# Performance work log

Hardware: AMD Instinct MI355X
Metric: run time of the kernel (lower is better)

The kernel has to match this reference:

```python
import jax, jax.numpy as jnp
import numpy as np

B, M, I = 32, 8192, 256
TEMPERATURE = 1.0


def setup_inputs() -> dict:
    key = jax.random.key(0)
    k1, k2, k3, k4 = jax.random.split(key, 4)
    memory = jax.random.normal(k1, (B, M, I), dtype=jnp.float32)
    qkey = jax.random.normal(k2, (B, I), dtype=jnp.float32)
    beta = jax.random.uniform(k3, (B,), dtype=jnp.float32)
    # xavier-uniform init for Linear(I, I)
    limit = float(np.sqrt(6.0 / (I + I)))
    W = jax.random.uniform(k4, (I, I), dtype=jnp.float32, minval=-limit, maxval=limit)
    b = jnp.zeros((I,), dtype=jnp.float32)
    return {"memory": memory, "key": qkey, "beta": beta, "W": W, "b": b}


def reference(memory, key, beta, W, b):
    # projected_key = tanh(key @ W^T + b)  -- torch Linear stores weight [out, in]
    projected_key = jnp.tanh(key @ W.T + b)                      # [B, I]
    diff = projected_key[:, None, :] - memory                    # [B, M, I]
    distances = jnp.sum(diff * diff, axis=-1)                    # [B, M]
    similarity = -distances
    weights = jax.nn.softmax(beta[:, None] * similarity / TEMPERATURE, axis=-1)  # [B, M]
    read_vector = jnp.einsum('bm,bmi->bi', weights, memory)      # [B, I]
    return weights, read_vector, similarity
```

## Files before the change

kernel.cpp:

```cpp
#include <hip/hip_runtime.h>
#include <math.h>

constexpr int Bdim = 32;
constexpr int Mdim = 8192;
constexpr int Idim = 256;
constexpr int ROWS_PER_BLOCK = 128;
constexpr int ROWS_PER_WAVE = 32;
constexpr int NCHUNK = Mdim / ROWS_PER_BLOCK;
constexpr int NSLICE = 8;

__global__ void proj_key_kernel(const float* __restrict__ key,
                                const float* __restrict__ W,
                                const float* __restrict__ bias,
                                float* __restrict__ pk) {
    int b = blockIdx.x >> 3;
    int slice = blockIdx.x & 7;
    int tid = threadIdx.x;
    int row = slice * 32 + (tid >> 3);
    int seg = tid & 7;

    const float4* w4 = (const float4*)(W + (size_t)row * Idim) + seg * 8;
    const float4* k4 = (const float4*)(key + (size_t)b * Idim) + seg * 8;
    float s = 0.f;
    #pragma unroll
    for (int k = 0; k < 8; ++k) {
        float4 wv = w4[k];
        float4 kv = k4[k];
        s += wv.x * kv.x + wv.y * kv.y + wv.z * kv.z + wv.w * kv.w;
    }
    s += __shfl_xor(s, 4, 64);
    s += __shfl_xor(s, 2, 64);
    s += __shfl_xor(s, 1, 64);
    if (seg == 0) pk[(size_t)b * Idim + row] = tanhf(s + bias[row]);
}

__global__ void fused_pass1_kernel(const float* __restrict__ memory,
                                   const float* __restrict__ pk,
                                   const float* __restrict__ beta,
                                   float* __restrict__ sim,
                                   float* __restrict__ pvec,
                                   float* __restrict__ pmx,
                                   float* __restrict__ psum) {
    int b = blockIdx.x / NCHUNK;
    int c = blockIdx.x % NCHUNK;
    int wave = threadIdx.x >> 6;
    int lane = threadIdx.x & 63;
    float bt = beta[b];

    float4 pkv = ((const float4*)(pk + (size_t)b * Idim))[lane];

    int row0 = c * ROWS_PER_BLOCK + wave * ROWS_PER_WAVE;
    const float* base = memory + ((size_t)b * Mdim + row0) * Idim;
    float* simp = sim + (size_t)b * Mdim + row0;

    float mx = -INFINITY, ssum = 0.f;
    float4 acc = make_float4(0.f, 0.f, 0.f, 0.f);
    float my_sim = 0.f;

    const float4* rp = (const float4*)base + lane;

    for (int g = 0; g < ROWS_PER_WAVE / 8; ++g) {
        float4 m[8];
        #pragma unroll
        for (int j = 0; j < 8; ++j)
            m[j] = rp[(size_t)(g * 8 + j) * 64];

        float s[8];
        #pragma unroll
        for (int j = 0; j < 8; ++j) {
            float dx = pkv.x - m[j].x, dy = pkv.y - m[j].y;
            float dz = pkv.z - m[j].z, dw = pkv.w - m[j].w;
            s[j] = dx * dx + dy * dy + dz * dz + dw * dw;
        }
        #pragma unroll
        for (int off = 32; off; off >>= 1) {
            #pragma unroll
            for (int j = 0; j < 8; ++j) s[j] += __shfl_xor(s[j], off, 64);
        }
        if ((lane >> 3) == g) my_sim = -s[lane & 7];

        #pragma unroll
        for (int j = 0; j < 8; ++j) s[j] = -bt * s[j];
        float gm = fmaxf(fmaxf(fmaxf(s[0], s[1]), fmaxf(s[2], s[3])),
                         fmaxf(fmaxf(s[4], s[5]), fmaxf(s[6], s[7])));
        if (gm > mx) {
            float sc = __expf(mx - gm);
            ssum *= sc;
            acc.x *= sc; acc.y *= sc; acc.z *= sc; acc.w *= sc;
            mx = gm;
        }
        float ps = 0.f;
        #pragma unroll
        for (int j = 0; j < 8; ++j) {
            float p = __expf(s[j] - mx);
            ps += p;
            acc.x = fmaf(p, m[j].x, acc.x);
            acc.y = fmaf(p, m[j].y, acc.y);
            acc.z = fmaf(p, m[j].z, acc.z);
            acc.w = fmaf(p, m[j].w, acc.w);
        }
        ssum += ps;
    }
    if (lane < 32) simp[lane] = my_sim;

    __shared__ float lacc[4][Idim];
    __shared__ float lmx[4], lsum[4];
    ((float4*)lacc[wave])[lane] = acc;
    if (lane == 0) { lmx[wave] = mx; lsum[wave] = ssum; }
    __syncthreads();

    float MX = fmaxf(fmaxf(lmx[0], lmx[1]), fmaxf(lmx[2], lmx[3]));
    float e0 = __expf(lmx[0] - MX), e1 = __expf(lmx[1] - MX);
    float e2 = __expf(lmx[2] - MX), e3 = __expf(lmx[3] - MX);
    int i = threadIdx.x;
    float v = lacc[0][i] * e0 + lacc[1][i] * e1 + lacc[2][i] * e2 + lacc[3][i] * e3;
    size_t pc = (size_t)b * NCHUNK + c;
    pvec[pc * Idim + i] = v;
    if (threadIdx.x == 0) {
        pmx[pc] = MX;
        psum[pc] = lsum[0] * e0 + lsum[1] * e1 + lsum[2] * e2 + lsum[3] * e3;
    }
}

__global__ void epilogue_kernel(const float* __restrict__ pvec,
                                const float* __restrict__ pmx,
                                const float* __restrict__ psum,
                                const float* __restrict__ sim,
                                const float* __restrict__ beta,
                                float* __restrict__ read_vec,
                                float* __restrict__ weights) {
    int b = blockIdx.x / NSLICE;
    int slice = blockIdx.x % NSLICE;
    int tid = threadIdx.x;
    __shared__ float e[NCHUNK];
    __shared__ float MXs, sInvs;

    if (tid < NCHUNK) {
        float m = pmx[(size_t)b * NCHUNK + tid];
        float mm = m;
        #pragma unroll
        for (int off = 32; off; off >>= 1) mm = fmaxf(mm, __shfl_xor(mm, off, 64));
        float ec = __expf(m - mm);
        e[tid] = ec;
        float sc = psum[(size_t)b * NCHUNK + tid] * ec;
        #pragma unroll
        for (int off = 32; off; off >>= 1) sc += __shfl_xor(sc, off, 64);
        if (tid == 0) { MXs = mm; sInvs = 1.f / sc; }
    }
    __syncthreads();

    float MX = MXs, inv = sInvs;

    if (slice == 0) {
        float v = 0.f;
        const float* p = pvec + (size_t)b * NCHUNK * Idim + tid;
        #pragma unroll 8
        for (int c = 0; c < NCHUNK; ++c) v += p[(size_t)c * Idim] * e[c];
        read_vec[(size_t)b * Idim + tid] = v * inv;
    }

    float bt = beta[b];
    int m4 = slice * (Mdim / NSLICE / 4) + tid;
    float4 s = ((const float4*)(sim + (size_t)b * Mdim))[m4];
    float4 w;
    w.x = __expf(bt * s.x - MX) * inv;
    w.y = __expf(bt * s.y - MX) * inv;
    w.z = __expf(bt * s.z - MX) * inv;
    w.w = __expf(bt * s.w - MX) * inv;
    ((float4*)(weights + (size_t)b * Mdim))[m4] = w;
}

extern "C" void kernel_launch(void* const* d_in, const int* in_sizes, int n_in,
                              void* d_out, int out_size, void* d_ws, size_t ws_size,
                              hipStream_t stream) {
    const float* memory = (const float*)d_in[0];
    const float* key    = (const float*)d_in[1];
    const float* beta   = (const float*)d_in[2];
    const float* W      = (const float*)d_in[3];
    const float* bias   = (const float*)d_in[4];

    float* out = (float*)d_out;
    float* weights  = out;
    float* read_vec = out + (size_t)Bdim * Mdim;
    float* sim      = read_vec + (size_t)Bdim * Idim;

    float* pk   = (float*)d_ws;
    float* pvec = pk + (size_t)Bdim * Idim;
    float* pmx  = pvec + (size_t)Bdim * NCHUNK * Idim;
    float* psum = pmx + (size_t)Bdim * NCHUNK;

    proj_key_kernel<<<Bdim * 8, 256, 0, stream>>>(key, W, bias, pk);
    fused_pass1_kernel<<<Bdim * NCHUNK, 256, 0, stream>>>(memory, pk, beta,
                                                          sim, pvec, pmx, psum);
    epilogue_kernel<<<Bdim * NSLICE, 256, 0, stream>>>(pvec, pmx, psum, sim, beta,
                                                       read_vec, weights);
}
```

Measured before the change: 53.90 us.

## Fuse softmax epilogue into main pass via last-block atomic counter

Merges the separate epilogue kernel into the main streaming kernel. Each block increments a per-batch atomic counter after writing its partials, and the last block for each batch performs the cross-chunk max/sum combine, the read vector, and the weights normalisation. This removes one kernel launch and its dependency gap. In exchange it adds a memset of the counters and serialises the weights tail onto 32 blocks instead of 256.

```diff
diff --git a/kernel.cpp b/kernel.cpp
--- a/kernel.cpp
+++ b/kernel.cpp
@@ -7,7 +7,6 @@
 constexpr int ROWS_PER_BLOCK = 128;
 constexpr int ROWS_PER_WAVE = 32;
 constexpr int NCHUNK = Mdim / ROWS_PER_BLOCK;
-constexpr int NSLICE = 8;
 
 __global__ void proj_key_kernel(const float* __restrict__ key,
                                 const float* __restrict__ W,
@@ -34,17 +33,21 @@
     if (seg == 0) pk[(size_t)b * Idim + row] = tanhf(s + bias[row]);
 }
 
-__global__ void fused_pass1_kernel(const float* __restrict__ memory,
-                                   const float* __restrict__ pk,
-                                   const float* __restrict__ beta,
-                                   float* __restrict__ sim,
-                                   float* __restrict__ pvec,
-                                   float* __restrict__ pmx,
-                                   float* __restrict__ psum) {
+__global__ void fused_kernel(const float* __restrict__ memory,
+                             const float* __restrict__ pk,
+                             const float* __restrict__ beta,
+                             float* __restrict__ sim,
+                             float* __restrict__ pvec,
+                             float* __restrict__ pmx,
+                             float* __restrict__ psum,
+                             float* __restrict__ read_vec,
+                             float* __restrict__ weights,
+                             unsigned int* __restrict__ cnt) {
     int b = blockIdx.x / NCHUNK;
     int c = blockIdx.x % NCHUNK;
-    int wave = threadIdx.x >> 6;
-    int lane = threadIdx.x & 63;
+    int tid = threadIdx.x;
+    int wave = tid >> 6;
+    int lane = tid & 63;
     float bt = beta[b];
 
     float4 pkv = ((const float4*)(pk + (size_t)b * Idim))[lane];
@@ -112,29 +115,27 @@
     float MX = fmaxf(fmaxf(lmx[0], lmx[1]), fmaxf(lmx[2], lmx[3]));
     float e0 = __expf(lmx[0] - MX), e1 = __expf(lmx[1] - MX);
     float e2 = __expf(lmx[2] - MX), e3 = __expf(lmx[3] - MX);
-    int i = threadIdx.x;
-    float v = lacc[0][i] * e0 + lacc[1][i] * e1 + lacc[2][i] * e2 + lacc[3][i] * e3;
+    float v = lacc[0][tid] * e0 + lacc[1][tid] * e1 +
+              lacc[2][tid] * e2 + lacc[3][tid] * e3;
     size_t pc = (size_t)b * NCHUNK + c;
-    pvec[pc * Idim + i] = v;
-    if (threadIdx.x == 0) {
+    pvec[pc * Idim + tid] = v;
+    if (tid == 0) {
         pmx[pc] = MX;
         psum[pc] = lsum[0] * e0 + lsum[1] * e1 + lsum[2] * e2 + lsum[3] * e3;
     }
-}
-
-__global__ void epilogue_kernel(const float* __restrict__ pvec,
-                                const float* __restrict__ pmx,
-                                const float* __restrict__ psum,
-                                const float* __restrict__ sim,
-                                const float* __restrict__ beta,
-                                float* __restrict__ read_vec,
-                                float* __restrict__ weights) {
-    int b = blockIdx.x / NSLICE;
-    int slice = blockIdx.x % NSLICE;
-    int tid = threadIdx.x;
+
+    __syncthreads();
+    __shared__ unsigned int is_last;
+    if (tid == 0) {
+        __threadfence();
+        is_last = (atomicAdd(&cnt[b], 1u) == NCHUNK - 1);
+    }
+    __syncthreads();
+    if (!is_last) return;
+    __threadfence();
+
     __shared__ float e[NCHUNK];
     __shared__ float MXs, sInvs;
-
     if (tid < NCHUNK) {
         float m = pmx[(size_t)b * NCHUNK + tid];
         float mm = m;
@@ -149,25 +150,26 @@
     }
     __syncthreads();
 
-    float MX = MXs, inv = sInvs;
-
-    if (slice == 0) {
-        float v = 0.f;
-        const float* p = pvec + (size_t)b * NCHUNK * Idim + tid;
-        #pragma unroll 8
-        for (int c = 0; c < NCHUNK; ++c) v += p[(size_t)c * Idim] * e[c];
-        read_vec[(size_t)b * Idim + tid] = v * inv;
-    }
-
-    float bt = beta[b];
-    int m4 = slice * (Mdim / NSLICE / 4) + tid;
-    float4 s = ((const float4*)(sim + (size_t)b * Mdim))[m4];
-    float4 w;
-    w.x = __expf(bt * s.x - MX) * inv;
-    w.y = __expf(bt * s.y - MX) * inv;
-    w.z = __expf(bt * s.z - MX) * inv;
-    w.w = __expf(bt * s.w - MX) * inv;
-    ((float4*)(weights + (size_t)b * Mdim))[m4] = w;
+    float gMX = MXs, inv = sInvs;
+
+    float rv = 0.f;
+    const float* p = pvec + (size_t)b * NCHUNK * Idim + tid;
+    #pragma unroll 8
+    for (int ch = 0; ch < NCHUNK; ++ch) rv += p[(size_t)ch * Idim] * e[ch];
+    read_vec[(size_t)b * Idim + tid] = rv * inv;
+
+    const float4* s4 = (const float4*)(sim + (size_t)b * Mdim);
+    float4* w4 = (float4*)(weights + (size_t)b * Mdim);
+    #pragma unroll
+    for (int m4 = tid; m4 < Mdim / 4; m4 += 256) {
+        float4 s = s4[m4];
+        float4 w;
+        w.x = __expf(bt * s.x - gMX) * inv;
+        w.y = __expf(bt * s.y - gMX) * inv;
+        w.z = __expf(bt * s.z - gMX) * inv;
+        w.w = __expf(bt * s.w - gMX) * inv;
+        w4[m4] = w;
+    }
 }
 
 extern "C" void kernel_launch(void* const* d_in, const int* in_sizes, int n_in,
@@ -188,10 +190,11 @@
     float* pvec = pk + (size_t)Bdim * Idim;
     float* pmx  = pvec + (size_t)Bdim * NCHUNK * Idim;
     float* psum = pmx + (size_t)Bdim * NCHUNK;
-
+    unsigned int* cnt = (unsigned int*)(psum + (size_t)Bdim * NCHUNK);
+
+    hipMemsetAsync(cnt, 0, Bdim * sizeof(unsigned int), stream);
     proj_key_kernel<<<Bdim * 8, 256, 0, stream>>>(key, W, bias, pk);
-    fused_pass1_kernel<<<Bdim * NCHUNK, 256, 0, stream>>>(memory, pk, beta,
-                                                          sim, pvec, pmx, psum);
-    epilogue_kernel<<<Bdim * NSLICE, 256, 0, stream>>>(pvec, pmx, psum, sim, beta,
-                                                       read_vec, weights);
+    fused_kernel<<<Bdim * NCHUNK, 256, 0, stream>>>(memory, pk, beta, sim,
+                                                    pvec, pmx, psum,
+                                                    read_vec, weights, cnt);
 }
```

Result: slower. 171.0 us (+217.3%).
